# Performance work log

Measured on AMD Instinct MI355X. Metric: run time of the kernel, lower is better.

## Reference

```python
import jax, jax.numpy as jnp
from jax import lax
import numpy as np

B, D, P, C = 16384, 256, 512, 20  # batch, input_dim, prototype_dim, n_class


def setup_inputs() -> dict:
    key = jax.random.key(0)
    k1, k2, k3 = jax.random.split(key, 3)
    return {
        "inputs": jax.random.normal(k1, (B, D), dtype=jnp.float32),
        "W": jax.random.normal(k2, (P, D), dtype=jnp.float32),
        "BETA": jax.random.normal(k3, (P, C), dtype=jnp.float32),
        "alpha": jnp.zeros((P, 1), dtype=jnp.float32),
        "gamma": jnp.full((P, 1), 0.1, dtype=jnp.float32),
        "n_class": C,
        "prototype_dim": P,
    }


def reference(inputs, W, BETA, alpha, gamma, n_class, prototype_dim):
    # inputs: [B, D], W: [P, D], BETA: [P, C], alpha/gamma: [P, 1]
    BETA2 = BETA * BETA
    U = BETA2 / BETA2.sum(axis=1, keepdims=True)          # [P, C]
    alphap = 0.99 / (1.0 + jnp.exp(-alpha))               # [P, 1]
    # d[k, b] = 0.5 * ||x_b - W_k||^2 via the expanded quadratic form
    d = 0.5 * (jnp.sum(W * W, axis=1)[:, None]
               + jnp.sum(inputs * inputs, axis=1)[None, :]
               - 2.0 * W @ inputs.T)                      # [P, B]
    expo = jnp.exp(-(gamma * gamma) * d)                  # [P, B]
    s = alphap * expo                                     # [P, B]

    bsz = inputs.shape[0]

    def step(mk, xs):
        # mk: [C+1, B] combined mass; xs = (U_k [C], s_k [B])
        Uk, sk = xs
        m_c = Uk[:, None] * sk[None, :]                   # [C, B] singleton masses
        m_n = 1.0 - sk                                    # [B]   mass on ignorance
        mk_c, mk_n = mk[:-1], mk[-1]
        new_c = mk_c * (m_c + m_n[None, :]) + m_c * mk_n[None, :]
        new_n = mk_n * m_n
        return jnp.concatenate([new_c, new_n[None, :]], axis=0), None

    mk0 = jnp.concatenate([jnp.zeros((n_class, bsz), dtype=inputs.dtype),
                           jnp.ones((1, bsz), dtype=inputs.dtype)], axis=0)
    mk, _ = lax.scan(step, mk0, (U, s))                   # sequential over P prototypes
    K = mk.sum(axis=0)                                    # [B]
    return (mk / K[None, :]).T                            # [B, C+1]
```

## Files before the change

kernel.cpp:

```cpp
#include <hip/hip_runtime.h>
#include <math.h>


#define NBATCH 16384
#define ND     256
#define NP     512
#define NCLS   20
#define OC     21

typedef short  short8  __attribute__((ext_vector_type(8)));
typedef short  short4v __attribute__((ext_vector_type(4)));
typedef unsigned short ushort8 __attribute__((ext_vector_type(8)));
typedef float  f32x16  __attribute__((ext_vector_type(16)));

#define OFF_PWH 0u
#define OFF_PWL 262144u
#define OFF_VS  524288u
#define OFF_WQ  (OFF_VS + 43008u)
#define OFF_AP  (OFF_WQ + 2048u)
#define OFF_G2  (OFF_AP + 2048u)
#define WS_NEED ((size_t)(OFF_G2 + 2048u))

__device__ __forceinline__ unsigned short f2bf_rn(float f) {
  unsigned int u = __float_as_uint(f);
  unsigned int r = (u + 0x7FFFu + ((u >> 16) & 1u)) >> 16;
  return (unsigned short)r;
}
__device__ __forceinline__ float bf2f(unsigned short h) {
  return __uint_as_float(((unsigned int)h) << 16);
}

__global__ __launch_bounds__(256)
void prep(const float* __restrict__ Wsrc, const float* __restrict__ BETA,
          const float* __restrict__ alpha, const float* __restrict__ gamma,
          unsigned short* __restrict__ dh, unsigned short* __restrict__ dl,
          float* __restrict__ sq, float* __restrict__ VS,
          float* __restrict__ AP, float* __restrict__ G2)
{
  const int bid = blockIdx.x;
  if (bid < 64) {
    const int tid = bid * 256 + threadIdx.x;
    const int row = tid >> 5, seg = tid & 31;
    const float4* s4 = (const float4*)(Wsrc + (size_t)row * ND + seg * 8);
    const float4 a = s4[0], b = s4[1];
    const float v[8] = {a.x, a.y, a.z, a.w, b.x, b.y, b.z, b.w};
    ushort8 hv, lv;
    float ssq = 0.f;
    #pragma unroll
    for (int j = 0; j < 8; ++j) {
      ssq = fmaf(v[j], v[j], ssq);
      const unsigned short hh = f2bf_rn(v[j]);
      hv[j] = hh;
      lv[j] = f2bf_rn(v[j] - bf2f(hh));
    }
    const int tile = row >> 5, m = row & 31, step = seg >> 1, r = seg & 1;
    const size_t cidx = (size_t)(tile * 16 + step) * 64 + m + 32 * r;
    *(ushort8*)(dh + cidx * 8) = hv;
    *(ushort8*)(dl + cidx * 8) = lv;
    #pragma unroll
    for (int off = 1; off < 32; off <<= 1) ssq += __shfl_xor(ssq, off, 64);
    if (seg == 0) sq[row] = ssq;
  } else {
    const int k = (bid - 64) * 256 + threadIdx.x;
    if (k >= NP) return;
    float bv[NCLS], bs = 0.f;
    #pragma unroll
    for (int c = 0; c < NCLS; ++c) { bv[c] = BETA[k * NCLS + c]; bs = fmaf(bv[c], bv[c], bs); }
    const float binv = 1.f / bs;
    #pragma unroll
    for (int c = 0; c < NCLS; ++c) VS[c * NP + k] = 1.f - bv[c] * bv[c] * binv;
    VS[NCLS * NP + k] = 1.f;
    AP[k] = 0.99f / (1.f + __expf(-alpha[k]));
    const float g = gamma[k];
    G2[k] = g * g;
  }
}

__global__ __launch_bounds__(512)
void evid_main(const float* __restrict__ X,
               const unsigned short* __restrict__ PWH, const unsigned short* __restrict__ PWL,
               const float* __restrict__ VS, const float* __restrict__ WQ,
               const float* __restrict__ AP, const float* __restrict__ G2,
               float* __restrict__ OUT)
{
  __shared__ __align__(16) short Ah[16384], Al[16384];
  __shared__ __align__(16) float sst[2][8192];
  __shared__ float xqs[64];

  const int t    = threadIdx.x;
  const int lane = t & 63;
  const int wv   = __builtin_amdgcn_readfirstlane(t >> 6);
  const int tile = blockIdx.x;
  const int bbase = tile * 64;
  const int sh = wv & 1, pg = wv >> 1;
  const int pl = lane & 31, h = lane >> 5;

  const short8* bH = (const short8*)PWH + (size_t)pg * 1024 + lane;
  const short8* bL = (const short8*)PWL + (size_t)pg * 1024 + lane;
  short8 wbh[4], wbl[4];
  #pragma unroll
  for (int p = 0; p < 4; ++p) { wbh[p] = bH[p * 64]; wbl[p] = bL[p * 64]; }

  {
    const int r  = t >> 3;
    const int sg = t & 7;
    const int rsh = r >> 5, rm = r & 31;
    const float* xrow = X + (size_t)(bbase + r) * ND;
    float ssq = 0.f;
    #pragma unroll
    for (int it = 0; it < 8; ++it) {
      const int c0 = it * 32 + sg * 4;
      const float4 v = *(const float4*)(xrow + c0);
      const float vv[4] = {v.x, v.y, v.z, v.w};
      short4v h4, l4;
      #pragma unroll
      for (int j = 0; j < 4; ++j) {
        ssq = fmaf(vv[j], vv[j], ssq);
        const unsigned short hh = f2bf_rn(vv[j]);
        h4[j] = (short)hh;
        l4[j] = (short)f2bf_rn(vv[j] - bf2f(hh));
      }
      const int step = c0 >> 4, half = (c0 >> 3) & 1, j0 = c0 & 7;
      const int base = (((rsh * 16 + step) * 64) + (rm + 32 * half)) * 8 + j0;
      *(short4v*)&Ah[base] = h4;
      *(short4v*)&Al[base] = l4;
    }
    ssq += __shfl_xor(ssq, 1, 64);
    ssq += __shfl_xor(ssq, 2, 64);
    ssq += __shfl_xor(ssq, 4, 64);
    if (sg == 0) xqs[r] = ssq;
  }
  __syncthreads();

  float xqv[16];
  #pragma unroll
  for (int rg = 0; rg < 16; ++rg)
    xqv[rg] = xqs[sh * 32 + (rg & 3) + 8 * (rg >> 2) + 4 * h];

  float Apc[OC];
  #pragma unroll
  for (int c = 0; c < OC; ++c) Apc[c] = 1.0f;

  #pragma unroll 1
  for (int chunk = 0; chunk < 4; ++chunk) {
    const int par = chunk & 1;
    float* sp = &sst[par][0];

    const int kp = chunk * 128 + pg * 32 + pl;
    const float wqk = WQ[kp], apk = AP[kp], g2k = G2[kp];

    f32x16 accA, accB, accC;
    #pragma unroll
    for (int i = 0; i < 16; ++i) { accA[i] = 0.f; accB[i] = 0.f; accC[i] = 0.f; }
    const short8* aH = (const short8*)Ah + (size_t)sh * 1024 + lane;
    const short8* aL = (const short8*)Al + (size_t)sh * 1024 + lane;
    #pragma unroll
    for (int step = 0; step < 16; ++step) {
      const short8 ah = aH[step * 64], al = aL[step * 64];
      const short8 bh = wbh[step & 3], bl = wbl[step & 3];
      if (step < 12) {
        wbh[step & 3] = bH[(step + 4) * 64];
        wbl[step & 3] = bL[(step + 4) * 64];
      }
      accA = __builtin_amdgcn_mfma_f32_32x32x16_bf16(ah, bh, accA, 0, 0, 0);
      accB = __builtin_amdgcn_mfma_f32_32x32x16_bf16(ah, bl, accB, 0, 0, 0);
      accC = __builtin_amdgcn_mfma_f32_32x32x16_bf16(al, bh, accC, 0, 0, 0);
    }

    #pragma unroll
    for (int rg = 0; rg < 16; ++rg) {
      const int   m  = (rg & 3) + 8 * (rg >> 2) + 4 * h;
      const int   b  = sh * 32 + m;
      const int   col = (pg * 32 + pl + 4 * m) & 127;
      const float dv = 0.5f * (wqk + xqv[rg]) - (accA[rg] + accB[rg] + accC[rg]);
      sp[b * 128 + col] = apk * __expf(-g2k * dv);
    }

    if (chunk < 3) {
      bH += 4096; bL += 4096;
      #pragma unroll
      for (int p = 0; p < 4; ++p) { wbh[p] = bH[p * 64]; wbl[p] = bL[p * 64]; }
    }

    __syncthreads();

    {
      const int kl = wv * 16;
      float sv[16];
      #pragma unroll
      for (int q = 0; q < 4; ++q) {
        const int col = (kl + 4 * (lane & 31) + 4 * q) & 127;
        *(float4*)&sv[4 * q] = *(const float4*)&sp[lane * 128 + col];
      }
      const float* vtab = VS + chunk * 128 + kl;
      for (int c = 0; c < OC; ++c) {
        const float* vp = vtab + (size_t)c * NP;
        float f[16];
        #pragma unroll
        for (int j = 0; j < 16; ++j) f[j] = fmaf(-sv[j], vp[j], 1.0f);
        const float p0 = (f[0] * f[1]) * (f[2] * f[3]);
        const float p1 = (f[4] * f[5]) * (f[6] * f[7]);
        const float p2 = (f[8] * f[9]) * (f[10] * f[11]);
        const float p3 = (f[12] * f[13]) * (f[14] * f[15]);
        Apc[c] *= (p0 * p1) * (p2 * p3);
      }
    }
  }

  __syncthreads();
  float* S = &sst[0][0];
  #pragma unroll
  for (int c = 0; c < OC; ++c) S[(wv * OC + c) * 64 + lane] = Apc[c];
  __syncthreads();
  float* R  = S + 11008;
  {
    const int b = t & 63, j = t >> 6;
    for (int c = j; c < OC; c += 8) {
      float p = S[c * 64 + b];
      #pragma unroll
      for (int w = 1; w < 8; ++w) p *= S[(w * OC + c) * 64 + b];
      R[c * 64 + b] = p;
    }
  }
  __syncthreads();
  float* kv = R + 1344;
  if (t < 64) {
    const float Nv = R[NCLS * 64 + t];
    float K = Nv;
    #pragma unroll
    for (int c = 0; c < NCLS; ++c) K += R[c * 64 + t] - Nv;
    kv[t] = 1.0f / K;
  }
  __syncthreads();
  for (int idx = t; idx < 64 * OC; idx += 512) {
    const int b = idx / OC, c = idx - b * OC;
    const float Nv = R[NCLS * 64 + b];
    const float ik = kv[b];
    OUT[(size_t)tile * 64 * OC + idx] = (c < NCLS) ? (R[c * 64 + b] - Nv) * ik : Nv * ik;
  }
}

#define TBF 64
#define TKF 64
#define DSL 64
#define LDX 68

__device__ __forceinline__ void fma4(const float4 a, const float4 b, float& d) {
  d = fmaf(a.x, b.x, d); d = fmaf(a.y, b.y, d);
  d = fmaf(a.z, b.z, d); d = fmaf(a.w, b.w, d);
}

__global__ __launch_bounds__(256)
void evid_fused(const float* __restrict__ X, const float* __restrict__ Wm,
                const float* __restrict__ BETA, const float* __restrict__ ALPHA,
                const float* __restrict__ GAMMA, float* __restrict__ OUT)
{
  __shared__ __align__(16) float xs[DSL][LDX], wsh[DSL][LDX], ssf[TKF][LDX], vs[OC][LDX];
  __shared__ float xq[TBF], wq[TKF], apch[TKF], g2ch[TKF];
  __shared__ float redx[4][TBF], redw[4][TKF];
  const int t = threadIdx.x, bbase = blockIdx.x * TBF;
  const int tb = t & 15, tk = t >> 4, srow = t >> 4, sdq = t & 15;
  const int cbf = t & 63, part = t >> 6;
  float Ap[OC];
  #pragma unroll
  for (int c = 0; c < OC; ++c) Ap[c] = 1.0f;
  float xqacc = 0.0f;
  for (int chunk = 0; chunk < 8; ++chunk) {
    const int k0 = chunk * TKF;
    __syncthreads();
    if (t < TKF) {
      const int k = k0 + t;
      float bsum = 0.0f;
      #pragma unroll
      for (int c = 0; c < NCLS; ++c) { const float bv = BETA[k*NCLS+c]; bsum = fmaf(bv, bv, bsum); }
      const float binv = 1.0f / bsum;
      #pragma unroll
      for (int c = 0; c < NCLS; ++c) { const float bv = BETA[k*NCLS+c]; vs[c][t] = 1.0f - bv*bv*binv; }
      vs[NCLS][t] = 1.0f;
      apch[t] = 0.99f / (1.0f + expf(-ALPHA[k]));
      const float gv = GAMMA[k]; g2ch[t] = gv * gv;
    }
    float acc[4][4] = {};
    float wqacc = 0.0f;
    for (int sl = 0; sl < 4; ++sl) {
      const int d0 = sl * DSL;
      __syncthreads();
      #pragma unroll
      for (int p = 0; p < 4; ++p) {
        const int r = srow + 16 * p;
        *(float4*)&xs [r][4*sdq] = *(const float4*)&X [(size_t)(bbase + r)*ND + d0 + 4*sdq];
        *(float4*)&wsh[r][4*sdq] = *(const float4*)&Wm[(size_t)(k0    + r)*ND + d0 + 4*sdq];
      }
      __syncthreads();
      #pragma unroll
      for (int m = 0; m < 4; ++m) {
        const float4 v = *(const float4*)&wsh[cbf][part*16 + 4*m];
        wqacc = fmaf(v.x,v.x, fmaf(v.y,v.y, fmaf(v.z,v.z, fmaf(v.w,v.w, wqacc))));
      }
      if (chunk == 0) {
        #pragma unroll
        for (int m = 0; m < 4; ++m) {
          const float4 v = *(const float4*)&xs[cbf][part*16 + 4*m];
          xqacc = fmaf(v.x,v.x, fmaf(v.y,v.y, fmaf(v.z,v.z, fmaf(v.w,v.w, xqacc))));
        }
      }
      #pragma unroll
      for (int dq = 0; dq < 16; ++dq) {
        const float4 xa0 = *(const float4*)&xs [tb +  0][4*dq];
        const float4 xa1 = *(const float4*)&xs [tb + 16][4*dq];
        const float4 xa2 = *(const float4*)&xs [tb + 32][4*dq];
        const float4 xa3 = *(const float4*)&xs [tb + 48][4*dq];
        const float4 wb0 = *(const float4*)&wsh[tk +  0][4*dq];
        const float4 wb1 = *(const float4*)&wsh[tk + 16][4*dq];
        const float4 wb2 = *(const float4*)&wsh[tk + 32][4*dq];
        const float4 wb3 = *(const float4*)&wsh[tk + 48][4*dq];
        fma4(xa0, wb0, acc[0][0]); fma4(xa0, wb1, acc[0][1]); fma4(xa0, wb2, acc[0][2]); fma4(xa0, wb3, acc[0][3]);
        fma4(xa1, wb0, acc[1][0]); fma4(xa1, wb1, acc[1][1]); fma4(xa1, wb2, acc[1][2]); fma4(xa1, wb3, acc[1][3]);
        fma4(xa2, wb0, acc[2][0]); fma4(xa2, wb1, acc[2][1]); fma4(xa2, wb2, acc[2][2]); fma4(xa2, wb3, acc[2][3]);
        fma4(xa3, wb0, acc[3][0]); fma4(xa3, wb1, acc[3][1]); fma4(xa3, wb2, acc[3][2]); fma4(xa3, wb3, acc[3][3]);
      }
    }
    redw[part][cbf] = wqacc;
    if (chunk == 0) redx[part][cbf] = xqacc;
    __syncthreads();
    if (t < TKF) {
      wq[t] = redw[0][t] + redw[1][t] + redw[2][t] + redw[3][t];
      if (chunk == 0) xq[t] = redx[0][t] + redx[1][t] + redx[2][t] + redx[3][t];
    }
    __syncthreads();
    #pragma unroll
    for (int j = 0; j < 4; ++j) {
      const int kj = tk + 16 * j;
      const float wqk = wq[kj], ap = apch[kj], g2 = g2ch[kj];
      #pragma unroll
      for (int i = 0; i < 4; ++i) {
        const int bi = tb + 16 * i;
        ssf[kj][bi] = ap * expf(-g2 * (0.5f*(wqk + xq[bi]) - acc[i][j]));
      }
    }
    __syncthreads();
    {
      float sv[16];
      #pragma unroll
      for (int m = 0; m < 16; ++m) sv[m] = ssf[16*part + m][cbf];
      #pragma unroll
      for (int c = 0; c < OC; ++c) {
        float a = Ap[c];
        #pragma unroll
        for (int mq = 0; mq < 4; ++mq) {
          const float4 vv = *(const float4*)&vs[c][16*part + 4*mq];
          const float t0 = fmaf(-sv[4*mq+0], vv.x, 1.0f);
          const float t1 = fmaf(-sv[4*mq+1], vv.y, 1.0f);
          const float t2 = fmaf(-sv[4*mq+2], vv.z, 1.0f);
          const float t3 = fmaf(-sv[4*mq+3], vv.w, 1.0f);
          a = a * ((t0*t1)*(t2*t3));
        }
        Ap[c] = a;
      }
    }
  }
  __syncthreads();
  if (part >= 2) {
    #pragma unroll
    for (int c = 0; c < OC; ++c) ssf[(part-2)*OC + c][cbf] = Ap[c];
  }
  __syncthreads();
  if (part < 2) {
    #pragma unroll
    for (int c = 0; c < OC; ++c) Ap[c] *= ssf[part*OC + c][cbf];
  }
  __syncthreads();
  if (part == 1) {
    #pragma unroll
    for (int c = 0; c < OC; ++c) ssf[c][cbf] = Ap[c];
  }
  __syncthreads();
  if (part == 0) {
    #pragma unroll
    for (int c = 0; c < OC; ++c) Ap[c] *= ssf[c][cbf];
    const float Nv = Ap[NCLS];
    float Ks = Nv;
    #pragma unroll
    for (int c = 0; c < NCLS; ++c) Ks += Ap[c] - Nv;
    const float invk = 1.0f / Ks;
    #pragma unroll
    for (int c = 0; c < NCLS; ++c) ssf[c][cbf] = (Ap[c] - Nv) * invk;
    ssf[NCLS][cbf] = Nv * invk;
  }
  __syncthreads();
  for (int idx = t; idx < TBF*OC; idx += 256) {
    const int b = idx / OC, c = idx - b*OC;
    OUT[(size_t)bbase*OC + idx] = ssf[c][b];
  }
}

extern "C" void kernel_launch(void* const* d_in, const int* in_sizes, int n_in,
                              void* d_out, int out_size, void* d_ws, size_t ws_size,
                              hipStream_t stream) {
  (void)in_sizes; (void)n_in; (void)out_size;
  const float* X     = (const float*)d_in[0];
  const float* Wm    = (const float*)d_in[1];
  const float* BETA  = (const float*)d_in[2];
  const float* ALPHA = (const float*)d_in[3];
  const float* GAMMA = (const float*)d_in[4];
  float* OUT = (float*)d_out;

  if (ws_size < WS_NEED) {
    hipLaunchKernelGGL(evid_fused, dim3(NBATCH/TBF), dim3(256), 0, stream,
                       X, Wm, BETA, ALPHA, GAMMA, OUT);
    return;
  }
  char* ws = (char*)d_ws;
  unsigned short* PWH = (unsigned short*)(ws + OFF_PWH);
  unsigned short* PWL = (unsigned short*)(ws + OFF_PWL);
  float* VS = (float*)(ws + OFF_VS);
  float* WQ = (float*)(ws + OFF_WQ);
  float* AP = (float*)(ws + OFF_AP);
  float* G2 = (float*)(ws + OFF_G2);

  hipLaunchKernelGGL(prep, dim3(66), dim3(256), 0, stream,
                     Wm, BETA, ALPHA, GAMMA, PWH, PWL, WQ, VS, AP, G2);
  hipLaunchKernelGGL(evid_main, dim3(NBATCH/64), dim3(512), 0, stream,
                     X, PWH, PWL, VS, WQ, AP, G2, OUT);
}
```

Before: 112.3 us.

## Split fused kernel into GEMM-to-workspace and separate product-combine kernels

When the workspace is large enough, the fused evid_main kernel is replaced by two kernels. gemm_s computes the split-bf16 MFMA distance GEMM and the exp activations for 32-row tiles and writes the full B×P activation matrix to global workspace. combine reads it back and does the per-class product reduction across prototypes with a tree multiply in registers. This aims to balance occupancy and let each phase be tuned on its own, at the cost of a 32MB round trip through HBM. The fp32 fallback kernel is removed, and the smaller-workspace path still runs evid_main.

```diff
diff --git a/kernel.cpp b/kernel.cpp
--- a/kernel.cpp
+++ b/kernel.cpp
@@ -16,10 +16,12 @@
 #define OFF_PWH 0u
 #define OFF_PWL 262144u
 #define OFF_VS  524288u
-#define OFF_WQ  (OFF_VS + 43008u)
-#define OFF_AP  (OFF_WQ + 2048u)
-#define OFF_G2  (OFF_AP + 2048u)
-#define WS_NEED ((size_t)(OFF_G2 + 2048u))
+#define OFF_WQ  567296u
+#define OFF_AP  569344u
+#define OFF_G2  571392u
+#define WS_SMALL 573440u
+#define OFF_SG  1048576u
+#define WS_BIG  ((size_t)(OFF_SG + 33554432u))
 
 __device__ __forceinline__ unsigned short f2bf_rn(float f) {
   unsigned int u = __float_as_uint(f);
@@ -77,6 +79,165 @@
 }
 
 __global__ __launch_bounds__(512)
+void gemm_s(const float* __restrict__ X,
+            const unsigned short* __restrict__ PWH, const unsigned short* __restrict__ PWL,
+            const float* __restrict__ WQ, const float* __restrict__ AP,
+            const float* __restrict__ G2, float* __restrict__ SG)
+{
+  __shared__ __align__(16) short Ah[8192], Al[8192];
+  __shared__ float xqs[32];
+
+  const int t    = threadIdx.x;
+  const int lane = t & 63;
+  const int wv   = __builtin_amdgcn_readfirstlane(t >> 6);
+  const int tile = blockIdx.x;
+  const int bbase = tile * 32;
+  const int pl = lane & 31, h = lane >> 5;
+
+  const short8* bH = (const short8*)PWH + (size_t)wv * 1024 + lane;
+  const short8* bL = (const short8*)PWL + (size_t)wv * 1024 + lane;
+  short8 wbh[4], wbl[4];
+  #pragma unroll
+  for (int p = 0; p < 4; ++p) { wbh[p] = bH[p * 64]; wbl[p] = bL[p * 64]; }
+
+  {
+    const int r  = t >> 4;
+    const int sg = t & 15;
+    const float* xrow = X + (size_t)(bbase + r) * ND;
+    float ssq = 0.f;
+    #pragma unroll
+    for (int it = 0; it < 4; ++it) {
+      const int c0 = it * 64 + sg * 4;
+      const float4 v = *(const float4*)(xrow + c0);
+      const float vv[4] = {v.x, v.y, v.z, v.w};
+      short4v h4, l4;
+      #pragma unroll
+      for (int j = 0; j < 4; ++j) {
+        ssq = fmaf(vv[j], vv[j], ssq);
+        const unsigned short hh = f2bf_rn(vv[j]);
+        h4[j] = (short)hh;
+        l4[j] = (short)f2bf_rn(vv[j] - bf2f(hh));
+      }
+      const int step = c0 >> 4, half = (c0 >> 3) & 1, j0 = c0 & 7;
+      const int base = (step * 64 + (r + 32 * half)) * 8 + j0;
+      *(short4v*)&Ah[base] = h4;
+      *(short4v*)&Al[base] = l4;
+    }
+    ssq += __shfl_xor(ssq, 1, 64);
+    ssq += __shfl_xor(ssq, 2, 64);
+    ssq += __shfl_xor(ssq, 4, 64);
+    ssq += __shfl_xor(ssq, 8, 64);
+    if (sg == 0) xqs[r] = ssq;
+  }
+  __syncthreads();
+
+  float xqv[16];
+  #pragma unroll
+  for (int rg = 0; rg < 16; ++rg)
+    xqv[rg] = xqs[(rg & 3) + 8 * (rg >> 2) + 4 * h];
+
+  #pragma unroll 1
+  for (int chunk = 0; chunk < 2; ++chunk) {
+    const int kp = chunk * 256 + wv * 32 + pl;
+    const float wqk = WQ[kp], apk = AP[kp], g2k = G2[kp];
+
+    f32x16 accA, accB, accC;
+    #pragma unroll
+    for (int i = 0; i < 16; ++i) { accA[i] = 0.f; accB[i] = 0.f; accC[i] = 0.f; }
+    const short8* aH = (const short8*)Ah + lane;
+    const short8* aL = (const short8*)Al + lane;
+    #pragma unroll
+    for (int step = 0; step < 16; ++step) {
+      const short8 ah = aH[step * 64], al = aL[step * 64];
+      const short8 bh = wbh[step & 3], bl = wbl[step & 3];
+      if (step < 12) {
+        wbh[step & 3] = bH[(step + 4) * 64];
+        wbl[step & 3] = bL[(step + 4) * 64];
+      }
+      accA = __builtin_amdgcn_mfma_f32_32x32x16_bf16(ah, bh, accA, 0, 0, 0);
+      accB = __builtin_amdgcn_mfma_f32_32x32x16_bf16(ah, bl, accB, 0, 0, 0);
+      accC = __builtin_amdgcn_mfma_f32_32x32x16_bf16(al, bh, accC, 0, 0, 0);
+    }
+    if (chunk < 1) {
+      bH += 8192; bL += 8192;
+      #pragma unroll
+      for (int p = 0; p < 4; ++p) { wbh[p] = bH[p * 64]; wbl[p] = bL[p * 64]; }
+    }
+
+    float* sgb = SG + (size_t)tile * 16384 + kp;
+    #pragma unroll
+    for (int rg = 0; rg < 16; ++rg) {
+      const int   m  = (rg & 3) + 8 * (rg >> 2) + 4 * h;
+      const float dv = 0.5f * (wqk + xqv[rg]) - (accA[rg] + accB[rg] + accC[rg]);
+      sgb[m * 512] = apk * __expf(-g2k * dv);
+    }
+  }
+}
+
+__global__ __launch_bounds__(512)
+void combine(const float* __restrict__ SG, const float* __restrict__ VS,
+             float* __restrict__ OUT)
+{
+  __shared__ float S[12160];
+
+  const int t    = threadIdx.x;
+  const int lane = t & 63;
+  const int wv   = __builtin_amdgcn_readfirstlane(t >> 6);
+  const int tile = blockIdx.x;
+  const int k0   = wv * 64;
+
+  const float* srow = SG + ((size_t)(tile * 2 + (lane >> 5)) * 16384)
+                         + (size_t)(lane & 31) * 512 + k0;
+  float sv[64];
+  #pragma unroll
+  for (int q = 0; q < 16; ++q)
+    *(float4*)&sv[4 * q] = *(const float4*)(srow + 4 * q);
+
+  float Apc[OC];
+  const float* vt = VS + k0;
+  for (int c = 0; c < OC; ++c) {
+    const float* vp = vt + (size_t)c * NP;
+    float f[64];
+    #pragma unroll
+    for (int j = 0; j < 64; ++j) f[j] = fmaf(-sv[j], vp[j], 1.0f);
+    #pragma unroll
+    for (int w = 32; w >= 1; w >>= 1)
+      for (int j = 0; j < w; ++j) f[j] *= f[j + w];
+    Apc[c] = f[0];
+  }
+
+  #pragma unroll
+  for (int c = 0; c < OC; ++c) S[(wv * OC + c) * 64 + lane] = Apc[c];
+  __syncthreads();
+  float* R = S + 10752;
+  {
+    const int b = t & 63, j = t >> 6;
+    for (int c = j; c < OC; c += 8) {
+      float p = S[c * 64 + b];
+      #pragma unroll
+      for (int w = 1; w < 8; ++w) p *= S[(w * OC + c) * 64 + b];
+      R[c * 64 + b] = p;
+    }
+  }
+  __syncthreads();
+  float* kv = R + 1344;
+  if (t < 64) {
+    const float Nv = R[NCLS * 64 + t];
+    float K = Nv;
+    #pragma unroll
+    for (int c = 0; c < NCLS; ++c) K += R[c * 64 + t] - Nv;
+    kv[t] = 1.0f / K;
+  }
+  __syncthreads();
+  for (int idx = t; idx < 64 * OC; idx += 512) {
+    const int b = idx / OC, c = idx - b * OC;
+    const float Nv = R[NCLS * 64 + b];
+    OUT[(size_t)tile * 64 * OC + idx] =
+        ((c < NCLS) ? (R[c * 64 + b] - Nv) : Nv) * kv[b];
+  }
+}
+
+__global__ __launch_bounds__(512)
 void evid_main(const float* __restrict__ X,
                const unsigned short* __restrict__ PWH, const unsigned short* __restrict__ PWL,
                const float* __restrict__ VS, const float* __restrict__ WQ,
@@ -145,7 +306,6 @@
   for (int chunk = 0; chunk < 4; ++chunk) {
     const int par = chunk & 1;
     float* sp = &sst[par][0];
-
     const int kp = chunk * 128 + pg * 32 + pl;
     const float wqk = WQ[kp], apk = AP[kp], g2k = G2[kp];
 
@@ -240,160 +400,6 @@
   }
 }
 
-#define TBF 64
-#define TKF 64
-#define DSL 64
-#define LDX 68
-
-__device__ __forceinline__ void fma4(const float4 a, const float4 b, float& d) {
-  d = fmaf(a.x, b.x, d); d = fmaf(a.y, b.y, d);
-  d = fmaf(a.z, b.z, d); d = fmaf(a.w, b.w, d);
-}
-
-__global__ __launch_bounds__(256)
-void evid_fused(const float* __restrict__ X, const float* __restrict__ Wm,
-                const float* __restrict__ BETA, const float* __restrict__ ALPHA,
-                const float* __restrict__ GAMMA, float* __restrict__ OUT)
-{
-  __shared__ __align__(16) float xs[DSL][LDX], wsh[DSL][LDX], ssf[TKF][LDX], vs[OC][LDX];
-  __shared__ float xq[TBF], wq[TKF], apch[TKF], g2ch[TKF];
-  __shared__ float redx[4][TBF], redw[4][TKF];
-  const int t = threadIdx.x, bbase = blockIdx.x * TBF;
-  const int tb = t & 15, tk = t >> 4, srow = t >> 4, sdq = t & 15;
-  const int cbf = t & 63, part = t >> 6;
-  float Ap[OC];
-  #pragma unroll
-  for (int c = 0; c < OC; ++c) Ap[c] = 1.0f;
-  float xqacc = 0.0f;
-  for (int chunk = 0; chunk < 8; ++chunk) {
-    const int k0 = chunk * TKF;
-    __syncthreads();
-    if (t < TKF) {
-      const int k = k0 + t;
-      float bsum = 0.0f;
-      #pragma unroll
-      for (int c = 0; c < NCLS; ++c) { const float bv = BETA[k*NCLS+c]; bsum = fmaf(bv, bv, bsum); }
-      const float binv = 1.0f / bsum;
-      #pragma unroll
-      for (int c = 0; c < NCLS; ++c) { const float bv = BETA[k*NCLS+c]; vs[c][t] = 1.0f - bv*bv*binv; }
-      vs[NCLS][t] = 1.0f;
-      apch[t] = 0.99f / (1.0f + expf(-ALPHA[k]));
-      const float gv = GAMMA[k]; g2ch[t] = gv * gv;
-    }
-    float acc[4][4] = {};
-    float wqacc = 0.0f;
-    for (int sl = 0; sl < 4; ++sl) {
-      const int d0 = sl * DSL;
-      __syncthreads();
-      #pragma unroll
-      for (int p = 0; p < 4; ++p) {
-        const int r = srow + 16 * p;
-        *(float4*)&xs [r][4*sdq] = *(const float4*)&X [(size_t)(bbase + r)*ND + d0 + 4*sdq];
-        *(float4*)&wsh[r][4*sdq] = *(const float4*)&Wm[(size_t)(k0    + r)*ND + d0 + 4*sdq];
-      }
-      __syncthreads();
-      #pragma unroll
-      for (int m = 0; m < 4; ++m) {
-        const float4 v = *(const float4*)&wsh[cbf][part*16 + 4*m];
-        wqacc = fmaf(v.x,v.x, fmaf(v.y,v.y, fmaf(v.z,v.z, fmaf(v.w,v.w, wqacc))));
-      }
-      if (chunk == 0) {
-        #pragma unroll
-        for (int m = 0; m < 4; ++m) {
-          const float4 v = *(const float4*)&xs[cbf][part*16 + 4*m];
-          xqacc = fmaf(v.x,v.x, fmaf(v.y,v.y, fmaf(v.z,v.z, fmaf(v.w,v.w, xqacc))));
-        }
-      }
-      #pragma unroll
-      for (int dq = 0; dq < 16; ++dq) {
-        const float4 xa0 = *(const float4*)&xs [tb +  0][4*dq];
-        const float4 xa1 = *(const float4*)&xs [tb + 16][4*dq];
-        const float4 xa2 = *(const float4*)&xs [tb + 32][4*dq];
-        const float4 xa3 = *(const float4*)&xs [tb + 48][4*dq];
-        const float4 wb0 = *(const float4*)&wsh[tk +  0][4*dq];
-        const float4 wb1 = *(const float4*)&wsh[tk + 16][4*dq];
-        const float4 wb2 = *(const float4*)&wsh[tk + 32][4*dq];
-        const float4 wb3 = *(const float4*)&wsh[tk + 48][4*dq];
-        fma4(xa0, wb0, acc[0][0]); fma4(xa0, wb1, acc[0][1]); fma4(xa0, wb2, acc[0][2]); fma4(xa0, wb3, acc[0][3]);
-        fma4(xa1, wb0, acc[1][0]); fma4(xa1, wb1, acc[1][1]); fma4(xa1, wb2, acc[1][2]); fma4(xa1, wb3, acc[1][3]);
-        fma4(xa2, wb0, acc[2][0]); fma4(xa2, wb1, acc[2][1]); fma4(xa2, wb2, acc[2][2]); fma4(xa2, wb3, acc[2][3]);
-        fma4(xa3, wb0, acc[3][0]); fma4(xa3, wb1, acc[3][1]); fma4(xa3, wb2, acc[3][2]); fma4(xa3, wb3, acc[3][3]);
-      }
-    }
-    redw[part][cbf] = wqacc;
-    if (chunk == 0) redx[part][cbf] = xqacc;
-    __syncthreads();
-    if (t < TKF) {
-      wq[t] = redw[0][t] + redw[1][t] + redw[2][t] + redw[3][t];
-      if (chunk == 0) xq[t] = redx[0][t] + redx[1][t] + redx[2][t] + redx[3][t];
-    }
-    __syncthreads();
-    #pragma unroll
-    for (int j = 0; j < 4; ++j) {
-      const int kj = tk + 16 * j;
-      const float wqk = wq[kj], ap = apch[kj], g2 = g2ch[kj];
-      #pragma unroll
-      for (int i = 0; i < 4; ++i) {
-        const int bi = tb + 16 * i;
-        ssf[kj][bi] = ap * expf(-g2 * (0.5f*(wqk + xq[bi]) - acc[i][j]));
-      }
-    }
-    __syncthreads();
-    {
-      float sv[16];
-      #pragma unroll
-      for (int m = 0; m < 16; ++m) sv[m] = ssf[16*part + m][cbf];
-      #pragma unroll
-      for (int c = 0; c < OC; ++c) {
-        float a = Ap[c];
-        #pragma unroll
-        for (int mq = 0; mq < 4; ++mq) {
-          const float4 vv = *(const float4*)&vs[c][16*part + 4*mq];
-          const float t0 = fmaf(-sv[4*mq+0], vv.x, 1.0f);
-          const float t1 = fmaf(-sv[4*mq+1], vv.y, 1.0f);
-          const float t2 = fmaf(-sv[4*mq+2], vv.z, 1.0f);
-          const float t3 = fmaf(-sv[4*mq+3], vv.w, 1.0f);
-          a = a * ((t0*t1)*(t2*t3));
-        }
-        Ap[c] = a;
-      }
-    }
-  }
-  __syncthreads();
-  if (part >= 2) {
-    #pragma unroll
-    for (int c = 0; c < OC; ++c) ssf[(part-2)*OC + c][cbf] = Ap[c];
-  }
-  __syncthreads();
-  if (part < 2) {
-    #pragma unroll
-    for (int c = 0; c < OC; ++c) Ap[c] *= ssf[part*OC + c][cbf];
-  }
-  __syncthreads();
-  if (part == 1) {
-    #pragma unroll
-    for (int c = 0; c < OC; ++c) ssf[c][cbf] = Ap[c];
-  }
-  __syncthreads();
-  if (part == 0) {
-    #pragma unroll
-    for (int c = 0; c < OC; ++c) Ap[c] *= ssf[c][cbf];
-    const float Nv = Ap[NCLS];
-    float Ks = Nv;
-    #pragma unroll
-    for (int c = 0; c < NCLS; ++c) Ks += Ap[c] - Nv;
-    const float invk = 1.0f / Ks;
-    #pragma unroll
-    for (int c = 0; c < NCLS; ++c) ssf[c][cbf] = (Ap[c] - Nv) * invk;
-    ssf[NCLS][cbf] = Nv * invk;
-  }
-  __syncthreads();
-  for (int idx = t; idx < TBF*OC; idx += 256) {
-    const int b = idx / OC, c = idx - b*OC;
-    OUT[(size_t)bbase*OC + idx] = ssf[c][b];
-  }
-}
-
 extern "C" void kernel_launch(void* const* d_in, const int* in_sizes, int n_in,
                               void* d_out, int out_size, void* d_ws, size_t ws_size,
                               hipStream_t stream) {
@@ -405,11 +411,6 @@
   const float* GAMMA = (const float*)d_in[4];
   float* OUT = (float*)d_out;
 
-  if (ws_size < WS_NEED) {
-    hipLaunchKernelGGL(evid_fused, dim3(NBATCH/TBF), dim3(256), 0, stream,
-                       X, Wm, BETA, ALPHA, GAMMA, OUT);
-    return;
-  }
   char* ws = (char*)d_ws;
   unsigned short* PWH = (unsigned short*)(ws + OFF_PWH);
   unsigned short* PWL = (unsigned short*)(ws + OFF_PWL);
@@ -420,6 +421,15 @@
 
   hipLaunchKernelGGL(prep, dim3(66), dim3(256), 0, stream,
                      Wm, BETA, ALPHA, GAMMA, PWH, PWL, WQ, VS, AP, G2);
-  hipLaunchKernelGGL(evid_main, dim3(NBATCH/64), dim3(512), 0, stream,
-                     X, PWH, PWL, VS, WQ, AP, G2, OUT);
-}
+
+  if (ws_size >= WS_BIG) {
+    float* SG = (float*)(ws + OFF_SG);
+    hipLaunchKernelGGL(gemm_s, dim3(NBATCH/32), dim3(512), 0, stream,
+                       X, PWH, PWL, WQ, AP, G2, SG);
+    hipLaunchKernelGGL(combine, dim3(NBATCH/64), dim3(512), 0, stream,
+                       SG, VS, OUT);
+  } else {
+    hipLaunchKernelGGL(evid_main, dim3(NBATCH/64), dim3(512), 0, stream,
+                       X, PWH, PWL, VS, WQ, AP, G2, OUT);
+  }
+}
```

Result: no change. 111.9 us (-0.4%).
